# Kernel optimization log

Measured on AMD Instinct MI355X. Metric: run time of the kernel, lower is better.

The kernel has to match this reference:

```python
import jax, jax.numpy as jnp
import numpy as np

N = 50000          # nodes
E = 800000         # edges
IN = 32            # in_channels (train_tensor.shape[1])
OUT = 256          # out_channels
K = 4              # Chebyshev order
LAMBDA_MAX = 2.0   # canonical lambda_max for sym-normalized Laplacian


def setup_inputs() -> dict:
    key = jax.random.key(0)
    ks = jax.random.split(key, 32)
    inp = {}
    inp["X"] = jax.random.normal(ks[0], (N, IN), jnp.float32)
    inp["edge_index"] = jax.random.randint(ks[1], (2, E), 0, N)
    inp["edge_weight"] = jax.random.uniform(ks[2], (E,), jnp.float32)
    inp["H"] = jax.random.normal(ks[3], (N, OUT), jnp.float32)
    inp["C"] = jax.random.normal(ks[4], (N, OUT), jnp.float32)
    i = 5
    s_in = float(np.sqrt(6.0 / (IN + OUT)))   # glorot for W_g
    s_ch = float(np.sqrt(1.0 / OUT))          # ChebConv linear init scale
    for g in ["i", "f", "c", "o"]:
        inp[f"W_{g}"] = jax.random.uniform(ks[i], (IN, OUT), jnp.float32, -s_in, s_in); i += 1
        inp[f"b_{g}"] = jnp.zeros((1, OUT), jnp.float32)
        inp[f"conv_{g}_w"] = jax.random.uniform(ks[i], (K, OUT, OUT), jnp.float32, -s_ch, s_ch); i += 1
        inp[f"conv_{g}_b"] = jnp.zeros((OUT,), jnp.float32)
    return inp


def _cheb_basis(H, edge_index, edge_weight, lam):
    """Chebyshev basis T_0(L~)H .. T_{K-1}(L~)H for the scaled sym Laplacian.
    L~ = (2/lam) * (I - D^{-1/2} A D^{-1/2}) - I  (PyG ChebConv.__norm__)."""
    n = H.shape[0]
    src, dst = edge_index[0], edge_index[1]
    deg = jax.ops.segment_sum(edge_weight, src, num_segments=n)
    dis = jnp.where(deg > 0, jax.lax.rsqrt(deg), 0.0)
    w = -(2.0 / lam) * dis[src] * edge_weight * dis[dst]   # scaled off-diagonal
    d = 2.0 / lam - 1.0                                     # scaled diagonal

    def prop(x):  # L~ @ x via edge scatter + diagonal
        return jax.ops.segment_sum(w[:, None] * x[src], dst, num_segments=n) + d * x

    Tx0 = H
    Tx1 = prop(Tx0)
    Tx2 = 2.0 * prop(Tx1) - Tx0
    Tx3 = 2.0 * prop(Tx2) - Tx1
    return jnp.stack([Tx0, Tx1, Tx2, Tx3])  # [K, N, OUT]


def reference(X, edge_index, edge_weight, H, C,
              W_i, b_i, conv_i_w, conv_i_b,
              W_f, b_f, conv_f_w, conv_f_b,
              W_c, b_c, conv_c_w, conv_c_b,
              W_o, b_o, conv_o_w, conv_o_b):
    # Shared Chebyshev basis of H (identical across the 4 gates)
    Tx = _cheb_basis(H, edge_index, edge_weight, LAMBDA_MAX)  # [K, N, OUT]

    def gate(Wg, bg, cw, cb):
        conv = jnp.einsum('knf,kfo->no', Tx, cw) + cb
        return X @ Wg + conv + bg

    I = jax.nn.sigmoid(gate(W_i, b_i, conv_i_w, conv_i_b))
    F = jax.nn.sigmoid(gate(W_f, b_f, conv_f_w, conv_f_b))
    T = jnp.tanh(gate(W_c, b_c, conv_c_w, conv_c_b))
    C_new = F * C + I * T
    O = jax.nn.sigmoid(gate(W_o, b_o, conv_o_w, conv_o_b))
    H_new = O * jnp.tanh(C_new)
    return (H_new, C_new)
```

## Files before the change

kernel.cpp:

```cpp
#include <hip/hip_runtime.h>
#include <math.h>

#define NN   50000
#define EE   800000
#define INC  32
#define OUTC 256
#define NKB  132

using bf16x8 = __attribute__((ext_vector_type(8))) short;
using u16x8  = __attribute__((ext_vector_type(8))) unsigned short;
using f32x4  = __attribute__((ext_vector_type(4))) float;

struct __align__(8) Edge { int s; float w; };

__device__ __forceinline__ unsigned short f2b(float f) {
  union { float f; unsigned u; } v; v.f = f;
  return (unsigned short)((v.u + 0x7FFFu + ((v.u >> 16) & 1u)) >> 16);
}
__device__ __forceinline__ float b2f(unsigned short u) {
  union { unsigned u; float f; } v; v.u = ((unsigned)u) << 16; return v.f;
}


__global__ void k_edge1(const int* __restrict__ ei, const float* __restrict__ ew,
                        float* __restrict__ deg, int* __restrict__ cnt) {
  for (int e = blockIdx.x * blockDim.x + threadIdx.x; e < EE;
       e += gridDim.x * blockDim.x) {
    atomicAdd(&deg[ei[e]], ew[e]);
    atomicAdd(&cnt[ei[EE + e]], 1);
  }
}

__global__ __launch_bounds__(512) void k_scan1(const int* __restrict__ cnt,
                                               int* __restrict__ row_ptr,
                                               int* __restrict__ bsum) {
  __shared__ int sd[512];
  int t = threadIdx.x;
  int i = blockIdx.x * 512 + t;
  int x = (i < NN) ? cnt[i] : 0;
  sd[t] = x;
  __syncthreads();
  for (int off = 1; off < 512; off <<= 1) {
    int v = (t >= off) ? sd[t - off] : 0;
    __syncthreads();
    sd[t] += v;
    __syncthreads();
  }
  if (i < NN) row_ptr[i] = sd[t] - x;
  if (t == 511) bsum[blockIdx.x] = sd[511];
}

__global__ __launch_bounds__(128) void k_scan2(int* __restrict__ bsum,
                                               int* __restrict__ row_ptr,
                                               int nblk) {
  __shared__ int sd[128];
  int t = threadIdx.x;
  int x = (t < nblk) ? bsum[t] : 0;
  sd[t] = x;
  __syncthreads();
  for (int off = 1; off < 128; off <<= 1) {
    int v = (t >= off) ? sd[t - off] : 0;
    __syncthreads();
    sd[t] += v;
    __syncthreads();
  }
  if (t < nblk) bsum[t] = sd[t] - x;
  if (t == 127) row_ptr[NN] = sd[127];
}

__global__ void k_scan3(int* __restrict__ row_ptr, const int* __restrict__ bsum,
                        int* __restrict__ nxt, float* __restrict__ deg) {
  int i = blockIdx.x * blockDim.x + threadIdx.x;
  if (i < NN) {
    int v = row_ptr[i] + bsum[i >> 9];
    row_ptr[i] = v;
    nxt[i] = v;
    float d = deg[i];
    deg[i] = d > 0.f ? rsqrtf(d) : 0.f;
  }
}

__global__ void k_fill(const int* __restrict__ ei, const float* __restrict__ ew,
                       const float* __restrict__ dis, int* __restrict__ nxt,
                       Edge* __restrict__ ev) {
  for (int e = blockIdx.x * blockDim.x + threadIdx.x; e < EE;
       e += gridDim.x * blockDim.x) {
    int s = ei[e], d = ei[EE + e];
    int pos = atomicAdd(&nxt[d], 1);
    Edge eg; eg.s = s; eg.w = -dis[s] * ew[e] * dis[d];
    ev[pos] = eg;
  }
}


__global__ __launch_bounds__(256) void k_prop_bf(
    const int* __restrict__ row_ptr, const Edge* __restrict__ ev,
    const unsigned short* __restrict__ xb,
    const unsigned short* __restrict__ initb, float scale,
    unsigned short* __restrict__ outb) {
  int wid = blockIdx.x * 4 + (threadIdx.x >> 6);
  if (wid >= NN) return;
  int lane = threadIdx.x & 63;
  int half = lane >> 5;
  int cl = lane & 31;
  int start = __builtin_amdgcn_readfirstlane(row_ptr[wid]);
  int end = __builtin_amdgcn_readfirstlane(row_ptr[wid + 1]);
  const size_t cofs = (size_t)(cl << 3);

  float a0[8], a1[8], a2[8], a3[8];
#pragma unroll
  for (int i = 0; i < 8; ++i) { a0[i] = 0.f; a1[i] = 0.f; a2[i] = 0.f; a3[i] = 0.f; }

  int j = start;
  for (; j + 7 < end; j += 8) {
    Edge e0 = ev[j + half];
    Edge e1 = ev[j + 2 + half];
    Edge e2 = ev[j + 4 + half];
    Edge e3 = ev[j + 6 + half];
    u16x8 u0 = *(const u16x8*)(xb + (size_t)e0.s * OUTC + cofs);
    u16x8 u1 = *(const u16x8*)(xb + (size_t)e1.s * OUTC + cofs);
    u16x8 u2 = *(const u16x8*)(xb + (size_t)e2.s * OUTC + cofs);
    u16x8 u3 = *(const u16x8*)(xb + (size_t)e3.s * OUTC + cofs);
#pragma unroll
    for (int i = 0; i < 8; ++i) {
      a0[i] = fmaf(e0.w, b2f(u0[i]), a0[i]);
      a1[i] = fmaf(e1.w, b2f(u1[i]), a1[i]);
      a2[i] = fmaf(e2.w, b2f(u2[i]), a2[i]);
      a3[i] = fmaf(e3.w, b2f(u3[i]), a3[i]);
    }
  }
  for (; j + 1 < end; j += 2) {
    Edge e0 = ev[j + half];
    u16x8 u0 = *(const u16x8*)(xb + (size_t)e0.s * OUTC + cofs);
#pragma unroll
    for (int i = 0; i < 8; ++i) a0[i] = fmaf(e0.w, b2f(u0[i]), a0[i]);
  }
  if (j < end) {
    Edge e0 = ev[j];
    float wv = half ? 0.f : e0.w;
    u16x8 u0 = *(const u16x8*)(xb + (size_t)e0.s * OUTC + cofs);
#pragma unroll
    for (int i = 0; i < 8; ++i) a0[i] = fmaf(wv, b2f(u0[i]), a0[i]);
  }

  float o[8];
#pragma unroll
  for (int i = 0; i < 8; ++i) {
    float s = (a0[i] + a1[i]) + (a2[i] + a3[i]);
    s += __shfl_xor(s, 32);
    o[i] = s;
  }
  if (initb) {
    u16x8 iv = *(const u16x8*)(initb + (size_t)wid * OUTC + cofs);
#pragma unroll
    for (int i = 0; i < 8; ++i) o[i] = scale * o[i] - b2f(iv[i]);
  }
  if (half == 1) {
    u16x8 h;
#pragma unroll
    for (int i = 0; i < 8; ++i) h[i] = f2b(o[i]);
    *(u16x8*)(outb + (size_t)wid * OUTC + cofs) = h;
  }
}


__global__ void k_packXH(const float* __restrict__ X, const float* __restrict__ H,
                         unsigned short* __restrict__ xrm,
                         unsigned short* __restrict__ hrm) {
  int t = blockIdx.x * blockDim.x + threadIdx.x;
  if (t < NN * 4) {
    int row = t >> 2, kb = t & 3;
    float4 a = *(const float4*)(X + (size_t)row * INC + kb * 8);
    float4 b = *(const float4*)(X + (size_t)row * INC + kb * 8 + 4);
    u16x8 h;
    h[0] = f2b(a.x); h[1] = f2b(a.y); h[2] = f2b(a.z); h[3] = f2b(a.w);
    h[4] = f2b(b.x); h[5] = f2b(b.y); h[6] = f2b(b.z); h[7] = f2b(b.w);
    *(u16x8*)(xrm + (size_t)row * INC + kb * 8) = h;
  } else if (t < NN * 36) {
    int u = t - NN * 4;
    int row = u >> 5, kb = u & 31;
    float4 a = *(const float4*)(H + (size_t)row * OUTC + kb * 8);
    float4 b = *(const float4*)(H + (size_t)row * OUTC + kb * 8 + 4);
    u16x8 h;
    h[0] = f2b(a.x); h[1] = f2b(a.y); h[2] = f2b(a.z); h[3] = f2b(a.w);
    h[4] = f2b(b.x); h[5] = f2b(b.y); h[6] = f2b(b.z); h[7] = f2b(b.w);
    *(u16x8*)(hrm + (size_t)row * OUTC + kb * 8) = h;
  }
}

struct BPtrs {
  const float* W[4];
  const float* cw[4];
  const float* b[4];
  const float* cb[4];
};

__global__ void k_packB(BPtrs bp, unsigned short* __restrict__ bpk,
                        float* __restrict__ bias_pk) {
  int t = blockIdx.x * blockDim.x + threadIdx.x;
  if (t >= NKB * 1024) return;
  int kb = t >> 10, p = t & 1023;
  int j = p >> 7, c = (p >> 6) & 1, g = (p >> 4) & 3, s = p & 15;
  int o = j * 32 + c * 16 + s;
  u16x8 h;
#pragma unroll
  for (int j8 = 0; j8 < 8; ++j8) {
    int k = kb * 8 + j8;
    float v = (k < 32) ? bp.W[g][k * OUTC + o]
                       : bp.cw[g][(size_t)(k - 32) * OUTC + o];
    h[j8] = f2b(v);
  }
  *(u16x8*)(bpk + (size_t)t * 8) = h;
  if (kb == 0) bias_pk[p] = bp.b[g][o] + bp.cb[g][o];
}


__device__ __forceinline__ float sigf(float x) {
  return __builtin_amdgcn_rcpf(1.0f + __expf(-x));
}
__device__ __forceinline__ float tanhfast(float x) {
  float e = __expf(2.0f * x);
  return 1.0f - 2.0f * __builtin_amdgcn_rcpf(e + 1.0f);
}

#define AS1(p) ((__attribute__((address_space(1))) void*)(p))
#define AS3(p) ((__attribute__((address_space(3))) void*)(p))

__global__ __launch_bounds__(256, 3) void k_gemm_mfma(
    const unsigned short* __restrict__ Xrm,
    const unsigned short* __restrict__ Hrm,
    const unsigned short* __restrict__ T1rm,
    const unsigned short* __restrict__ T2rm,
    const unsigned short* __restrict__ T3rm,
    const unsigned short* __restrict__ Bpk,
    const float* __restrict__ bias_pk,
    const float* __restrict__ C,
    float* __restrict__ Hn, float* __restrict__ Cn) {
  __shared__ unsigned short Als[3][128 * 4 * 8];

  const int b = blockIdx.x;
  const int xcd = b & 7;
  const int slot = b >> 3;
  const int cgrp = slot & 7;
  const int rblk = xcd + ((slot >> 3) << 3);
  const int bm0 = rblk * 128;
  if (bm0 >= NN) return;
  const int cb0 = cgrp * 128;

  const int tid = threadIdx.x;
  const int lane = tid & 63;
  const int wid = tid >> 6;
  const int wr = wid >> 1;
  const int wc = wid & 1;

  f32x4 acc[4][4];
#pragma unroll
  for (int i = 0; i < 4; ++i)
#pragma unroll
    for (int j = 0; j < 4; ++j) acc[i][j] = (f32x4){0.f, 0.f, 0.f, 0.f};

  const int sr = lane >> 2;
  const int scs = (lane & 3) ^ ((sr >> 1) & 3);
  int arow0 = bm0 + (wid << 5) + sr;
  int arow1 = arow0 + 16;
  if (arow0 > NN - 1) arow0 = NN - 1;
  if (arow1 > NN - 1) arow1 = NN - 1;
  const size_t rowA32_0 = (size_t)arow0 * INC + ((size_t)scs << 3);
  const size_t rowA32_1 = (size_t)arow1 * INC + ((size_t)scs << 3);
  const size_t rowA256_0 = (size_t)arow0 * OUTC + ((size_t)scs << 3);
  const size_t rowA256_1 = (size_t)arow1 * OUTC + ((size_t)scs << 3);

  const int koff = lane >> 4;
  const int r15 = lane & 15;
  const unsigned short* bGr =
      Bpk + ((size_t)koff * 1024 + cb0 + (wc << 6) + r15) * 8;

  auto STAGE_A = [&](int buf, int tile) {
    size_t o0, o1;
    const unsigned short* base;
    if (tile == 0)      { base = Xrm;  o0 = rowA32_0;  o1 = rowA32_1; }
    else if (tile < 9)  { base = Hrm;  o0 = rowA256_0 + (size_t)(tile - 1) * 32;
                          o1 = rowA256_1 + (size_t)(tile - 1) * 32; }
    else if (tile < 17) { base = T1rm; o0 = rowA256_0 + (size_t)(tile - 9) * 32;
                          o1 = rowA256_1 + (size_t)(tile - 9) * 32; }
    else if (tile < 25) { base = T2rm; o0 = rowA256_0 + (size_t)(tile - 17) * 32;
                          o1 = rowA256_1 + (size_t)(tile - 17) * 32; }
    else                { base = T3rm; o0 = rowA256_0 + (size_t)(tile - 25) * 32;
                          o1 = rowA256_1 + (size_t)(tile - 25) * 32; }
    __builtin_amdgcn_global_load_lds(AS1(base + o0),
                                     AS3(&Als[buf][(wid << 5) * 32]), 16, 0, 0);
    __builtin_amdgcn_global_load_lds(AS1(base + o1),
                                     AS3(&Als[buf][((wid << 5) + 16) * 32]), 16, 0, 0);
  };

  const int NT = NKB / 4;

  STAGE_A(0, 0);
  STAGE_A(1, 1);
  int cur = 0;
  for (int t = 0; t < NT; ++t) {
    asm volatile("s_waitcnt vmcnt(2)\n\ts_barrier" ::: "memory");

    const unsigned short* bt = bGr + (size_t)t * 32768;
    bf16x8 bf0 = *(const bf16x8*)(bt);
    bf16x8 bf1 = *(const bf16x8*)(bt + 128);
    bf16x8 bf2 = *(const bf16x8*)(bt + 256);
    bf16x8 bf3 = *(const bf16x8*)(bt + 384);

    if (t + 2 < NT) STAGE_A((t + 2) % 3, t + 2);

    const int row0 = (wr << 6) + r15;
    const int asw = (r15 >> 1) & 3;
    const unsigned short* Ab = &Als[cur][row0 * 32 + ((koff ^ asw) << 3)];
    bf16x8 af0 = *(const bf16x8*)(Ab);
    bf16x8 af1 = *(const bf16x8*)(Ab + 512);
    bf16x8 af2 = *(const bf16x8*)(Ab + 1024);
    bf16x8 af3 = *(const bf16x8*)(Ab + 1536);

    if (t + 2 < NT)
      asm volatile("s_waitcnt vmcnt(2) lgkmcnt(0)" ::: "memory");
    else
      asm volatile("s_waitcnt vmcnt(0) lgkmcnt(0)" ::: "memory");
    __builtin_amdgcn_sched_barrier(0);
    __builtin_amdgcn_s_setprio(1);
#define MM(m, n, bfn) acc[m][n] = __builtin_amdgcn_mfma_f32_16x16x32_bf16(af##m, bfn, acc[m][n], 0, 0, 0)
    MM(0, 0, bf0); MM(1, 0, bf0); MM(2, 0, bf0); MM(3, 0, bf0);
    MM(0, 1, bf1); MM(1, 1, bf1); MM(2, 1, bf1); MM(3, 1, bf1);
    MM(0, 2, bf2); MM(1, 2, bf2); MM(2, 2, bf2); MM(3, 2, bf2);
    MM(0, 3, bf3); MM(1, 3, bf3); MM(2, 3, bf3); MM(3, 3, bf3);
#undef MM
    __builtin_amdgcn_s_setprio(0);

    cur = (cur + 1 == 3) ? 0 : cur + 1;
  }

  const int ocol = cgrp * 32 + (wc << 4) + r15;
  float bz[4];
#pragma unroll
  for (int g = 0; g < 4; ++g) bz[g] = bias_pk[cb0 + (wc << 6) + (g << 4) + r15];

#pragma unroll
  for (int mi = 0; mi < 4; ++mi) {
    int rowb = bm0 + (wr << 6) + (mi << 4) + ((lane >> 4) << 2);
#pragma unroll
    for (int q = 0; q < 4; ++q) {
      int r = rowb + q;
      if (r >= NN) continue;
      float zi = acc[mi][0][q] + bz[0];
      float zf = acc[mi][1][q] + bz[1];
      float zc = acc[mi][2][q] + bz[2];
      float zo = acc[mi][3][q] + bz[3];
      float cold = C[(size_t)r * OUTC + ocol];
      float I = sigf(zi), F = sigf(zf), T = tanhfast(zc), O = sigf(zo);
      float cn = fmaf(F, cold, I * T);
      Cn[(size_t)r * OUTC + ocol] = cn;
      Hn[(size_t)r * OUTC + ocol] = O * tanhfast(cn);
    }
  }
}


extern "C" void kernel_launch(void* const* d_in, const int* in_sizes, int n_in,
                              void* d_out, int out_size, void* d_ws, size_t ws_size,
                              hipStream_t stream) {
  const float* X = (const float*)d_in[0];
  const int* EI = (const int*)d_in[1];
  const float* EW = (const float*)d_in[2];
  const float* H = (const float*)d_in[3];
  const float* C = (const float*)d_in[4];

  char* ws = (char*)d_ws;
  size_t off = 0;
  auto alloc = [&](size_t bytes) -> void* {
    void* p = ws + off;
    off += (bytes + 255) & ~(size_t)255;
    return p;
  };
  int* row_ptr = (int*)alloc((NN + 1) * sizeof(int));
  int* cnt = (int*)alloc(NN * sizeof(int));
  int* nextp = (int*)alloc(NN * sizeof(int));
  int* bsum = (int*)alloc(128 * sizeof(int));
  Edge* ev = (Edge*)alloc(EE * sizeof(Edge));
  float* dis = (float*)alloc(NN * sizeof(float));
  unsigned short* Xrm = (unsigned short*)alloc((size_t)NN * INC * sizeof(unsigned short));
  unsigned short* Hrm = (unsigned short*)alloc((size_t)NN * OUTC * sizeof(unsigned short));
  unsigned short* T1rm = (unsigned short*)alloc((size_t)NN * OUTC * sizeof(unsigned short));
  unsigned short* T2rm = (unsigned short*)alloc((size_t)NN * OUTC * sizeof(unsigned short));
  unsigned short* T3rm = (unsigned short*)alloc((size_t)NN * OUTC * sizeof(unsigned short));
  unsigned short* Bpk = (unsigned short*)alloc((size_t)NKB * 1024 * 8 * sizeof(unsigned short));
  float* bias_pk = (float*)alloc(1024 * sizeof(float));
  (void)ws_size; (void)in_sizes; (void)n_in; (void)out_size;

  hipMemsetAsync(dis, 0, NN * sizeof(float), stream);
  hipMemsetAsync(cnt, 0, NN * sizeof(int), stream);

  const int ge = 1024;
  k_edge1<<<ge, 256, 0, stream>>>(EI, EW, dis, cnt);
  const int nscb = (NN + 511) / 512;
  k_scan1<<<nscb, 512, 0, stream>>>(cnt, row_ptr, bsum);
  k_scan2<<<1, 128, 0, stream>>>(bsum, row_ptr, nscb);
  k_scan3<<<(NN + 255) / 256, 256, 0, stream>>>(row_ptr, bsum, nextp, dis);
  k_fill<<<ge, 256, 0, stream>>>(EI, EW, dis, nextp, ev);

  k_packXH<<<(NN * 36 + 255) / 256, 256, 0, stream>>>(X, H, Xrm, Hrm);
  BPtrs bp;
  for (int g = 0; g < 4; ++g) {
    bp.W[g] = (const float*)d_in[5 + 4 * g];
    bp.b[g] = (const float*)d_in[6 + 4 * g];
    bp.cw[g] = (const float*)d_in[7 + 4 * g];
    bp.cb[g] = (const float*)d_in[8 + 4 * g];
  }
  k_packB<<<(NKB * 1024 + 255) / 256, 256, 0, stream>>>(bp, Bpk, bias_pk);

  const int pgrid = (NN + 3) / 4;
  k_prop_bf<<<pgrid, 256, 0, stream>>>(row_ptr, ev, Hrm, nullptr, 1.f, T1rm);
  k_prop_bf<<<pgrid, 256, 0, stream>>>(row_ptr, ev, T1rm, Hrm, 2.f, T2rm);
  k_prop_bf<<<pgrid, 256, 0, stream>>>(row_ptr, ev, T2rm, T1rm, 2.f, T3rm);

  float* Hn = (float*)d_out;
  float* Cn = (float*)d_out + (size_t)NN * OUTC;
  k_gemm_mfma<<<8 * 49 * 8, 256, 0, stream>>>(Xrm, Hrm, T1rm, T2rm, T3rm,
                                              Bpk, bias_pk, C, Hn, Cn);
}
```

Before: 511.7 us.

## Give each wave a private LDS A-tile and prefetch B fragments to drop barriers

The GEMM main loop is restructured so each wave stages its own 64-row A slice into a private LDS region (4 loads per wave), which removes the block-wide s_barrier per k-tile. B fragments are double-buffered in registers (p/q) and loaded one tile ahead, with the loop unrolled by two. This aims to cut synchronisation stalls and hide global-load latency. The cost is duplicated A loads, since both column-waves in a row now fetch the same rows, more vmcnt bookkeeping, higher register pressure at 3 blocks per CU, and a larger LDS footprint.

```diff
diff --git a/kernel.cpp b/kernel.cpp
--- a/kernel.cpp
+++ b/kernel.cpp
@@ -236,7 +236,7 @@
     const float* __restrict__ bias_pk,
     const float* __restrict__ C,
     float* __restrict__ Hn, float* __restrict__ Cn) {
-  __shared__ unsigned short Als[3][128 * 4 * 8];
+  __shared__ unsigned short Als[4][3][64 * 32];
 
   const int b = blockIdx.x;
   const int xcd = b & 7;
@@ -261,14 +261,12 @@
 
   const int sr = lane >> 2;
   const int scs = (lane & 3) ^ ((sr >> 1) & 3);
-  int arow0 = bm0 + (wid << 5) + sr;
-  int arow1 = arow0 + 16;
-  if (arow0 > NN - 1) arow0 = NN - 1;
-  if (arow1 > NN - 1) arow1 = NN - 1;
-  const size_t rowA32_0 = (size_t)arow0 * INC + ((size_t)scs << 3);
-  const size_t rowA32_1 = (size_t)arow1 * INC + ((size_t)scs << 3);
-  const size_t rowA256_0 = (size_t)arow0 * OUTC + ((size_t)scs << 3);
-  const size_t rowA256_1 = (size_t)arow1 * OUTC + ((size_t)scs << 3);
+  int arow[4];
+#pragma unroll
+  for (int g = 0; g < 4; ++g) {
+    int r = bm0 + (wr << 6) + (g << 4) + sr;
+    arow[g] = (r > NN - 1) ? (NN - 1) : r;
+  }
 
   const int koff = lane >> 4;
   const int r15 = lane & 15;
@@ -276,63 +274,85 @@
       Bpk + ((size_t)koff * 1024 + cb0 + (wc << 6) + r15) * 8;
 
   auto STAGE_A = [&](int buf, int tile) {
-    size_t o0, o1;
     const unsigned short* base;
-    if (tile == 0)      { base = Xrm;  o0 = rowA32_0;  o1 = rowA32_1; }
-    else if (tile < 9)  { base = Hrm;  o0 = rowA256_0 + (size_t)(tile - 1) * 32;
-                          o1 = rowA256_1 + (size_t)(tile - 1) * 32; }
-    else if (tile < 17) { base = T1rm; o0 = rowA256_0 + (size_t)(tile - 9) * 32;
-                          o1 = rowA256_1 + (size_t)(tile - 9) * 32; }
-    else if (tile < 25) { base = T2rm; o0 = rowA256_0 + (size_t)(tile - 17) * 32;
-                          o1 = rowA256_1 + (size_t)(tile - 17) * 32; }
-    else                { base = T3rm; o0 = rowA256_0 + (size_t)(tile - 25) * 32;
-                          o1 = rowA256_1 + (size_t)(tile - 25) * 32; }
-    __builtin_amdgcn_global_load_lds(AS1(base + o0),
-                                     AS3(&Als[buf][(wid << 5) * 32]), 16, 0, 0);
-    __builtin_amdgcn_global_load_lds(AS1(base + o1),
-                                     AS3(&Als[buf][((wid << 5) + 16) * 32]), 16, 0, 0);
+    size_t rstride, cofs;
+    if (tile == 0)      { base = Xrm;  rstride = INC;  cofs = 0; }
+    else if (tile < 9)  { base = Hrm;  rstride = OUTC; cofs = (size_t)(tile - 1) * 32; }
+    else if (tile < 17) { base = T1rm; rstride = OUTC; cofs = (size_t)(tile - 9) * 32; }
+    else if (tile < 25) { base = T2rm; rstride = OUTC; cofs = (size_t)(tile - 17) * 32; }
+    else                { base = T3rm; rstride = OUTC; cofs = (size_t)(tile - 25) * 32; }
+#pragma unroll
+    for (int g = 0; g < 4; ++g) {
+      __builtin_amdgcn_global_load_lds(
+          AS1(base + (size_t)arow[g] * rstride + cofs + ((size_t)scs << 3)),
+          AS3(&Als[wid][buf][(g << 4) * 32]), 16, 0, 0);
+    }
   };
 
-  const int NT = NKB / 4;
+  bf16x8 p0, p1, p2, p3, q0, q1, q2, q3;
+#define LOADB(d0, d1, d2, d3, t)                                   \
+  { const unsigned short* bt = bGr + (size_t)(t) * 32768;          \
+    d0 = *(const bf16x8*)(bt);       d1 = *(const bf16x8*)(bt + 128); \
+    d2 = *(const bf16x8*)(bt + 256); d3 = *(const bf16x8*)(bt + 384); }
+
+  const int asw = (r15 >> 1) & 3;
+#define READA(buf)                                                     \
+  const unsigned short* Ab = &Als[wid][buf][r15 * 32 + ((koff ^ asw) << 3)]; \
+  bf16x8 af0 = *(const bf16x8*)(Ab);                                   \
+  bf16x8 af1 = *(const bf16x8*)(Ab + 512);                             \
+  bf16x8 af2 = *(const bf16x8*)(Ab + 1024);                            \
+  bf16x8 af3 = *(const bf16x8*)(Ab + 1536);
+
+#define MFMA16(B0, B1, B2, B3)                                                      \
+  acc[0][0] = __builtin_amdgcn_mfma_f32_16x16x32_bf16(af0, B0, acc[0][0], 0, 0, 0); \
+  acc[1][0] = __builtin_amdgcn_mfma_f32_16x16x32_bf16(af1, B0, acc[1][0], 0, 0, 0); \
+  acc[2][0] = __builtin_amdgcn_mfma_f32_16x16x32_bf16(af2, B0, acc[2][0], 0, 0, 0); \
+  acc[3][0] = __builtin_amdgcn_mfma_f32_16x16x32_bf16(af3, B0, acc[3][0], 0, 0, 0); \
+  acc[0][1] = __builtin_amdgcn_mfma_f32_16x16x32_bf16(af0, B1, acc[0][1], 0, 0, 0); \
+  acc[1][1] = __builtin_amdgcn_mfma_f32_16x16x32_bf16(af1, B1, acc[1][1], 0, 0, 0); \
+  acc[2][1] = __builtin_amdgcn_mfma_f32_16x16x32_bf16(af2, B1, acc[2][1], 0, 0, 0); \
+  acc[3][1] = __builtin_amdgcn_mfma_f32_16x16x32_bf16(af3, B1, acc[3][1], 0, 0, 0); \
+  acc[0][2] = __builtin_amdgcn_mfma_f32_16x16x32_bf16(af0, B2, acc[0][2], 0, 0, 0); \
+  acc[1][2] = __builtin_amdgcn_mfma_f32_16x16x32_bf16(af1, B2, acc[1][2], 0, 0, 0); \
+  acc[2][2] = __builtin_amdgcn_mfma_f32_16x16x32_bf16(af2, B2, acc[2][2], 0, 0, 0); \
+  acc[3][2] = __builtin_amdgcn_mfma_f32_16x16x32_bf16(af3, B2, acc[3][2], 0, 0, 0); \
+  acc[0][3] = __builtin_amdgcn_mfma_f32_16x16x32_bf16(af0, B3, acc[0][3], 0, 0, 0); \
+  acc[1][3] = __builtin_amdgcn_mfma_f32_16x16x32_bf16(af1, B3, acc[1][3], 0, 0, 0); \
+  acc[2][3] = __builtin_amdgcn_mfma_f32_16x16x32_bf16(af2, B3, acc[2][3], 0, 0, 0); \
+  acc[3][3] = __builtin_amdgcn_mfma_f32_16x16x32_bf16(af3, B3, acc[3][3], 0, 0, 0);
 
   STAGE_A(0, 0);
+  LOADB(p0, p1, p2, p3, 0);
   STAGE_A(1, 1);
-  int cur = 0;
-  for (int t = 0; t < NT; ++t) {
-    asm volatile("s_waitcnt vmcnt(2)\n\ts_barrier" ::: "memory");
-
-    const unsigned short* bt = bGr + (size_t)t * 32768;
-    bf16x8 bf0 = *(const bf16x8*)(bt);
-    bf16x8 bf1 = *(const bf16x8*)(bt + 128);
-    bf16x8 bf2 = *(const bf16x8*)(bt + 256);
-    bf16x8 bf3 = *(const bf16x8*)(bt + 384);
-
-    if (t + 2 < NT) STAGE_A((t + 2) % 3, t + 2);
-
-    const int row0 = (wr << 6) + r15;
-    const int asw = (r15 >> 1) & 3;
-    const unsigned short* Ab = &Als[cur][row0 * 32 + ((koff ^ asw) << 3)];
-    bf16x8 af0 = *(const bf16x8*)(Ab);
-    bf16x8 af1 = *(const bf16x8*)(Ab + 512);
-    bf16x8 af2 = *(const bf16x8*)(Ab + 1024);
-    bf16x8 af3 = *(const bf16x8*)(Ab + 1536);
-
-    if (t + 2 < NT)
-      asm volatile("s_waitcnt vmcnt(2) lgkmcnt(0)" ::: "memory");
-    else
-      asm volatile("s_waitcnt vmcnt(0) lgkmcnt(0)" ::: "memory");
-    __builtin_amdgcn_sched_barrier(0);
-    __builtin_amdgcn_s_setprio(1);
-#define MM(m, n, bfn) acc[m][n] = __builtin_amdgcn_mfma_f32_16x16x32_bf16(af##m, bfn, acc[m][n], 0, 0, 0)
-    MM(0, 0, bf0); MM(1, 0, bf0); MM(2, 0, bf0); MM(3, 0, bf0);
-    MM(0, 1, bf1); MM(1, 1, bf1); MM(2, 1, bf1); MM(3, 1, bf1);
-    MM(0, 2, bf2); MM(1, 2, bf2); MM(2, 2, bf2); MM(3, 2, bf2);
-    MM(0, 3, bf3); MM(1, 3, bf3); MM(2, 3, bf3); MM(3, 3, bf3);
-#undef MM
-    __builtin_amdgcn_s_setprio(0);
-
-    cur = (cur + 1 == 3) ? 0 : cur + 1;
-  }
+
+  int c0 = 0;
+  for (int t = 0; t < 32; t += 2) {
+    const int c1 = (c0 + 1 == 3) ? 0 : c0 + 1;
+    const int c2 = (c1 + 1 == 3) ? 0 : c1 + 1;
+    asm volatile("s_waitcnt vmcnt(4)" ::: "memory");
+    LOADB(q0, q1, q2, q3, t + 1);
+    STAGE_A(c2, t + 2);
+    {
+      READA(c0);
+      MFMA16(p0, p1, p2, p3);
+    }
+    asm volatile("s_waitcnt vmcnt(4)" ::: "memory");
+    LOADB(p0, p1, p2, p3, t + 2);
+    if (t + 3 < 33) STAGE_A(c0, t + 3);
+    {
+      READA(c1);
+      MFMA16(q0, q1, q2, q3);
+    }
+    c0 = c2;
+  }
+  asm volatile("s_waitcnt vmcnt(0)" ::: "memory");
+  {
+    READA(2);
+    MFMA16(p0, p1, p2, p3);
+  }
+#undef MFMA16
+#undef READA
+#undef LOADB
 
   const int ocol = cgrp * 32 + (wc << 4) + r15;
   float bz[4];
```

After: 539.9 us. 5.5% more time.
